# Kernel tuning notes

Hardware: AMD Instinct MI355X
Metric: run time of the kernel (lower is better)

Reference implementation:

```python
import jax, jax.numpy as jnp
import numpy as np

B, N, D = 2, 2048, 1024
H = 16
HD = D // H  # 64
ROPE_BASE = 10000.0


def setup_inputs() -> dict:
    key = jax.random.key(0)
    ks = jax.random.split(key, 5)
    s = 0.02
    return {
        "x": jax.random.normal(ks[0], (B, N, D), dtype=jnp.float32),
        "qkv_w": jax.random.normal(ks[1], (3 * D, D), dtype=jnp.float32) * s,
        "qkv_b": jax.random.normal(ks[2], (3 * D,), dtype=jnp.float32) * s,
        "proj_w": jax.random.normal(ks[3], (D, D), dtype=jnp.float32) * s,
        "proj_b": jax.random.normal(ks[4], (D,), dtype=jnp.float32) * s,
    }


def _rotate_half(t):
    # interleaved pairs: (x1,x2) -> (-x2,x1), matching lucidrains RotaryEmbedding
    t = t.reshape(*t.shape[:-1], -1, 2)
    x1, x2 = t[..., 0], t[..., 1]
    return jnp.stack((-x2, x1), axis=-1).reshape(*t.shape[:-2], -1)


def _apply_rope(t, cos, sin):
    # t: [B, H, N, HD]; cos/sin: [N, HD]
    return t * cos + _rotate_half(t) * sin


def reference(x, qkv_w, qkv_b, proj_w, proj_b):
    b, n, d = x.shape
    scale = HD ** -0.5

    qkv = x @ qkv_w.T + qkv_b                      # [B, N, 3D]
    qkv = qkv.reshape(b, n, 3, H, HD)
    qkv = jnp.transpose(qkv, (2, 0, 3, 1, 4))       # [3, B, H, N, HD]
    q, k, v = qkv[0], qkv[1], qkv[2]

    # RoPE (lang freqs, interpolate_factor=1)
    inv_freq = 1.0 / (ROPE_BASE ** (jnp.arange(0, HD, 2, dtype=jnp.float32) / HD))
    freqs = jnp.arange(n, dtype=jnp.float32)[:, None] * inv_freq[None, :]  # [N, HD/2]
    freqs = jnp.repeat(freqs, 2, axis=-1)           # [N, HD] interleaved
    cos, sin = jnp.cos(freqs), jnp.sin(freqs)
    q = _apply_rope(q, cos, sin)
    k = _apply_rope(k, cos, sin)

    scores = jnp.einsum('bhid,bhjd->bhij', q, k) * scale  # [B, H, N, N]
    causal = jnp.triu(jnp.ones((n, n), dtype=bool), k=1)
    scores = jnp.where(causal, -jnp.inf, scores)
    attn = jax.nn.softmax(scores, axis=-1)

    out = jnp.einsum('bhij,bhjd->bhid', attn, v)    # [B, H, N, HD]
    out = jnp.transpose(out, (0, 2, 1, 3)).reshape(b, n, d)
    return out @ proj_w.T + proj_b
```

## Files before the change

### kernel.cpp

```cpp
#include <hip/hip_runtime.h>
#include <hip/hip_bf16.h>
#include <cstdint>
#include <cstddef>

typedef __hip_bfloat16 bf16;
typedef short bf16x8 __attribute__((ext_vector_type(8)));
typedef float f32x4 __attribute__((ext_vector_type(4)));
typedef float f32x16 __attribute__((ext_vector_type(16)));
typedef int i32x4 __attribute__((ext_vector_type(4)));

#define MFMA16(a, b, c) __builtin_amdgcn_mfma_f32_16x16x32_bf16((a), (b), (c), 0, 0, 0)
#define MFMA32(a, b, c) __builtin_amdgcn_mfma_f32_32x32x16_bf16((a), (b), (c), 0, 0, 0)

__device__ __forceinline__ void glds16(const bf16* g, bf16* l)
{
    __builtin_amdgcn_global_load_lds(
        (const __attribute__((address_space(1))) void*)g,
        (__attribute__((address_space(3))) void*)l, 16, 0, 0);
}

__device__ __forceinline__ unsigned pkbf16(float a, float b)
{
    bf16 ba = __float2bfloat16(a), bb = __float2bfloat16(b);
    unsigned ua = *reinterpret_cast<unsigned short*>(&ba);
    unsigned ub = *reinterpret_cast<unsigned short*>(&bb);
    return ua | (ub << 16);
}

__global__ void cvt_f32_bf16(const float* __restrict__ in, bf16* __restrict__ out, int n4)
{
    int i = blockIdx.x * blockDim.x + threadIdx.x;
    if (i >= n4) return;
    float4 v = *reinterpret_cast<const float4*>(in + (size_t)i * 4);
    __align__(8) bf16 tmp[4];
    tmp[0] = __float2bfloat16(v.x);
    tmp[1] = __float2bfloat16(v.y);
    tmp[2] = __float2bfloat16(v.z);
    tmp[3] = __float2bfloat16(v.w);
    *reinterpret_cast<short4*>(out + (size_t)i * 4) = *reinterpret_cast<short4*>(tmp);
}

__global__ void rope_table_kernel(float2* __restrict__ tab)
{
    int i = blockIdx.x * blockDim.x + threadIdx.x;
    int pos = i >> 5, f = i & 31;
    float inv = powf(10000.f, -(float)f * (1.f / 32.f));
    float ang = (float)pos * inv;
    tab[i] = make_float2(cosf(ang), sinf(ang));
}

__global__ void rope_apply_kernel(bf16* __restrict__ qkv, const float2* __restrict__ tab)
{
    int idx = blockIdx.x * blockDim.x + threadIdx.x;
    int row = idx >> 8;
    int cc  = (idx & 255) * 8;
    int pos = row & 2047;
    int hd  = cc & 63;
    bf16* p = qkv + (size_t)row * 3072 + cc;
    i32x4 v = *reinterpret_cast<const i32x4*>(p);
    bf16* e = reinterpret_cast<bf16*>(&v);
    const float2* tb = tab + pos * 32 + (hd >> 1);
#pragma unroll
    for (int pp = 0; pp < 4; ++pp) {
        float2 cs = tb[pp];
        float x1 = __bfloat162float(e[2 * pp]);
        float x2 = __bfloat162float(e[2 * pp + 1]);
        e[2 * pp]     = __float2bfloat16(x1 * cs.x - x2 * cs.y);
        e[2 * pp + 1] = __float2bfloat16(x2 * cs.x + x1 * cs.y);
    }
    *reinterpret_cast<i32x4*>(p) = v;
}

__device__ inline void store_out(float* p, float v) { *p = v; }
__device__ inline void store_out(bf16* p, float v) { *p = __float2bfloat16(v); }

template <typename OutT>
__global__ void gemm_bt_kernel(const bf16* __restrict__ A, const bf16* __restrict__ BT,
                               const float* __restrict__ bias, OutT* __restrict__ C,
                               int M, int N, int K)
{
    constexpr int BM = 128, BN = 128, BK = 32;
    __shared__ __align__(16) bf16 Al[BM * BK];
    __shared__ __align__(16) bf16 Bl[BN * BK];

    const int tid = threadIdx.x;
    const int l = tid & 63;
    const int w = tid >> 6;
    const int wr = w >> 1, wc = w & 1;
    const int l15 = l & 15, lhi = l >> 4;
    const int row0 = blockIdx.x * BM, col0 = blockIdx.y * BN;

    const int ar0 = tid >> 2, ar1 = (tid + 256) >> 2;
    const int ac  = (tid & 3) * 8;
    const bf16* Ag0 = A + (size_t)(row0 + ar0) * K + ac;
    const bf16* Ag1 = A + (size_t)(row0 + ar1) * K + ac;
    const bf16* Bg0 = BT + (size_t)(col0 + ar0) * K + ac;
    const bf16* Bg1 = BT + (size_t)(col0 + ar1) * K + ac;
    const int wbase = (tid & 192) * 8;
    bf16* sA0 = &Al[wbase];
    bf16* sA1 = &Al[2048 + wbase];
    bf16* sB0 = &Bl[wbase];
    bf16* sB1 = &Bl[2048 + wbase];

    f32x4 acc[4][4] = {};

    for (int k0 = 0; k0 < K; k0 += BK) {
        __syncthreads();
        glds16(Ag0 + k0, sA0);
        glds16(Ag1 + k0, sA1);
        glds16(Bg0 + k0, sB0);
        glds16(Bg1 + k0, sB1);
        __syncthreads();
        bf16x8 af[4], bfr[4];
#pragma unroll
        for (int m = 0; m < 4; ++m)
            af[m] = *reinterpret_cast<const bf16x8*>(&Al[(wr * 64 + m * 16 + l15) * BK + lhi * 8]);
#pragma unroll
        for (int n = 0; n < 4; ++n)
            bfr[n] = *reinterpret_cast<const bf16x8*>(&Bl[(wc * 64 + n * 16 + l15) * BK + lhi * 8]);
#pragma unroll
        for (int m = 0; m < 4; ++m)
#pragma unroll
            for (int n = 0; n < 4; ++n)
                acc[m][n] = MFMA16(af[m], bfr[n], acc[m][n]);
    }

#pragma unroll
    for (int m = 0; m < 4; ++m) {
#pragma unroll
        for (int n = 0; n < 4; ++n) {
            int col = col0 + wc * 64 + n * 16 + l15;
            float bs = bias[col];
#pragma unroll
            for (int j = 0; j < 4; ++j) {
                int row = row0 + wr * 64 + m * 16 + lhi * 4 + j;
                store_out(&C[(size_t)row * N + col], acc[m][n][j] + bs);
            }
        }
    }
}

__global__ __launch_bounds__(128, 2)
void attn_kernel(const bf16* __restrict__ qkv, bf16* __restrict__ outp)
{
    constexpr int LDK = 68, LDV = 68;
    __shared__ __align__(16) bf16 Kl[2][64 * LDK];
    __shared__ __align__(16) bf16 Vt[2][64 * LDV];
    __shared__ float wred[2][32];

    const int bh = blockIdx.x;
    const int b = bh >> 4, h = bh & 15;
    const int q0b = (31 - (int)blockIdx.y) * 64;
    const int tid = threadIdx.x;
    const int w = tid >> 6, l = tid & 63;
    const int q31 = l & 31, hi = l >> 5;
    const int q0w = q0b + w * 32;
    const int qa = q0w + q31;

    const size_t RS = 3072;
    const bf16* base = qkv + (size_t)b * 2048 * RS;

    bf16x8 qf[4];
    {
        const bf16* qr = base + (size_t)qa * RS + h * 64 + hi * 8;
#pragma unroll
        for (int s = 0; s < 4; ++s) {
            bf16x8 v = *reinterpret_cast<const bf16x8*>(qr + s * 16);
            bf16* e = reinterpret_cast<bf16*>(&v);
#pragma unroll
            for (int j = 0; j < 8; ++j)
                e[j] = __float2bfloat16(__bfloat162float(e[j]) * 0.18033688f);
            qf[s] = v;
        }
    }

    const int kr  = tid >> 2;
    const int kc  = (tid & 3) * 16;
    const bf16* kp = base + (size_t)kr * RS + 1024 + h * 64 + kc;
    const bf16* vp = base + (size_t)(w * 32) * RS + 2048 + h * 64 + l;

    i32x4 ka0, ka1, ka2, ka3;
    __align__(16) bf16 vt32[32];

    ka0 = *reinterpret_cast<const i32x4*>(kp);
    ka1 = *reinterpret_cast<const i32x4*>(kp + 8);
    ka2 = *reinterpret_cast<const i32x4*>(kp + 32 * RS);
    ka3 = *reinterpret_cast<const i32x4*>(kp + 32 * RS + 8);
#pragma unroll
    for (int j = 0; j < 32; ++j) vt32[j] = vp[(size_t)j * RS];
    *reinterpret_cast<i32x4*>(&Kl[0][kr * LDK + kc])            = ka0;
    *reinterpret_cast<i32x4*>(&Kl[0][kr * LDK + kc + 8])        = ka1;
    *reinterpret_cast<i32x4*>(&Kl[0][(kr + 32) * LDK + kc])     = ka2;
    *reinterpret_cast<i32x4*>(&Kl[0][(kr + 32) * LDK + kc + 8]) = ka3;
#pragma unroll
    for (int c = 0; c < 4; ++c)
        *reinterpret_cast<i32x4*>(&Vt[0][l * LDV + w * 32 + c * 8]) =
            *reinterpret_cast<const i32x4*>(&vt32[c * 8]);
    __syncthreads();

    float m_run = -1e30f, l_run = 0.f;
    f32x16 o0 = {}, o1 = {};

    const int ntiles = q0b / 64 + 1;
    int cur = 0;
    for (int t = 0; t < ntiles; ++t) {
        const int kv0 = t * 64;
        const bool pf = (t + 1 < ntiles);
        if (pf) {
            kp += 64 * RS;
            vp += 64 * RS;
            ka0 = *reinterpret_cast<const i32x4*>(kp);
            ka1 = *reinterpret_cast<const i32x4*>(kp + 8);
            ka2 = *reinterpret_cast<const i32x4*>(kp + 32 * RS);
            ka3 = *reinterpret_cast<const i32x4*>(kp + 32 * RS + 8);
#pragma unroll
            for (int j = 0; j < 32; ++j) vt32[j] = vp[(size_t)j * RS];
        }

        if (kv0 <= q0w + 31) {
            const bf16* Kc = &Kl[cur][0];
            const bf16* Vc = &Vt[cur][0];

            f32x16 p0 = {}, p1 = {};
#pragma unroll
            for (int s = 0; s < 4; ++s) {
                bf16x8 kf0 = *reinterpret_cast<const bf16x8*>(&Kc[q31 * LDK + s * 16 + hi * 8]);
                bf16x8 kf1 = *reinterpret_cast<const bf16x8*>(&Kc[(32 + q31) * LDK + s * 16 + hi * 8]);
                p0 = MFMA32(kf0, qf[s], p0);
                p1 = MFMA32(kf1, qf[s], p1);
            }

            if (kv0 + 63 > q0w) {
                const int lim = qa - kv0 - 4 * hi;
#pragma unroll
                for (int r = 0; r < 16; ++r) {
                    const int cr = (r & 3) + 8 * (r >> 2);
                    if (cr > lim)      p0[r] = -1e30f;
                    if (cr + 32 > lim) p1[r] = -1e30f;
                }
            }

            float rm = p0[0];
#pragma unroll
            for (int r = 1; r < 16; ++r) rm = fmaxf(rm, p0[r]);
#pragma unroll
            for (int r = 0; r < 16; ++r) rm = fmaxf(rm, p1[r]);
            rm = fmaxf(rm, __shfl_xor(rm, 32));

            if (!__all(rm - m_run <= 8.0f)) {
                float mnew = fmaxf(m_run, rm);
                float alpha = exp2f(m_run - mnew);
                m_run = mnew;
                l_run *= alpha;
                if (hi == 0) wred[w][q31] = alpha;
#pragma unroll
                for (int g = 0; g < 4; ++g) {
                    f32x4 av = *reinterpret_cast<const f32x4*>(&wred[w][8 * g + 4 * hi]);
#pragma unroll
                    for (int tt = 0; tt < 4; ++tt) {
                        o0[4 * g + tt] *= av[tt];
                        o1[4 * g + tt] *= av[tt];
                    }
                }
            }

            float rsum = 0.f;
#pragma unroll
            for (int r = 0; r < 16; ++r) { p0[r] = exp2f(p0[r] - m_run); rsum += p0[r]; }
#pragma unroll
            for (int r = 0; r < 16; ++r) { p1[r] = exp2f(p1[r] - m_run); rsum += p1[r]; }
            rsum += __shfl_xor(rsum, 32);
            l_run += rsum;

            unsigned A[8], Bv[8];
#pragma unroll
            for (int m = 0; m < 4; ++m) {
                A[m]      = pkbf16(p0[4 * m],     p0[4 * m + 1]);
                Bv[m]     = pkbf16(p0[4 * m + 2], p0[4 * m + 3]);
                A[m + 4]  = pkbf16(p1[4 * m],     p1[4 * m + 1]);
                Bv[m + 4] = pkbf16(p1[4 * m + 2], p1[4 * m + 3]);
            }

#pragma unroll
            for (int ks = 0; ks < 4; ++ks) {
                unsigned sa = hi ? A[2 * ks]  : A[2 * ks + 1];
                unsigned sb = hi ? Bv[2 * ks] : Bv[2 * ks + 1];
                unsigned ra = (unsigned)__shfl_xor((int)sa, 32);
                unsigned rb = (unsigned)__shfl_xor((int)sb, 32);
                union { unsigned u[4]; bf16x8 v; } pa;
                if (hi == 0) { pa.u[0] = A[2 * ks];  pa.u[1] = Bv[2 * ks];  pa.u[2] = ra; pa.u[3] = rb; }
                else         { pa.u[0] = ra; pa.u[1] = rb; pa.u[2] = A[2 * ks + 1]; pa.u[3] = Bv[2 * ks + 1]; }
                bf16x8 vf0 = *reinterpret_cast<const bf16x8*>(&Vc[q31 * LDV + ks * 16 + hi * 8]);
                bf16x8 vf1 = *reinterpret_cast<const bf16x8*>(&Vc[(32 + q31) * LDV + ks * 16 + hi * 8]);
                o0 = MFMA32(pa.v, vf0, o0);
                o1 = MFMA32(pa.v, vf1, o1);
            }
        }

        if (pf) {
            const int nxt = cur ^ 1;
            *reinterpret_cast<i32x4*>(&Kl[nxt][kr * LDK + kc])            = ka0;
            *reinterpret_cast<i32x4*>(&Kl[nxt][kr * LDK + kc + 8])        = ka1;
            *reinterpret_cast<i32x4*>(&Kl[nxt][(kr + 32) * LDK + kc])     = ka2;
            *reinterpret_cast<i32x4*>(&Kl[nxt][(kr + 32) * LDK + kc + 8]) = ka3;
#pragma unroll
            for (int c = 0; c < 4; ++c)
                *reinterpret_cast<i32x4*>(&Vt[nxt][l * LDV + w * 32 + c * 8]) =
                    *reinterpret_cast<const i32x4*>(&vt32[c * 8]);
            __syncthreads();
            cur = nxt;
        }
    }

    if (hi == 0) wred[w][q31] = 1.0f / l_run;
#pragma unroll
    for (int g = 0; g < 4; ++g) {
        f32x4 iv = *reinterpret_cast<const f32x4*>(&wred[w][8 * g + 4 * hi]);
#pragma unroll
        for (int tt = 0; tt < 4; ++tt) {
            const int r = 4 * g + tt;
            const int qrow = q0w + 8 * g + 4 * hi + tt;
            bf16* op = outp + (size_t)(b * 2048 + qrow) * 1024 + h * 64 + q31;
            op[0]  = __float2bfloat16(o0[r] * iv[tt]);
            op[32] = __float2bfloat16(o1[r] * iv[tt]);
        }
    }
}

extern "C" void kernel_launch(void* const* d_in, const int* in_sizes, int n_in,
                              void* d_out, int out_size, void* d_ws, size_t ws_size,
                              hipStream_t stream)
{
    const float* x      = (const float*)d_in[0];
    const float* qkv_w  = (const float*)d_in[1];
    const float* qkv_b  = (const float*)d_in[2];
    const float* proj_w = (const float*)d_in[3];
    const float* proj_b = (const float*)d_in[4];
    float* out = (float*)d_out;

    char* ws = (char*)d_ws;
    bf16* x_bf   = (bf16*)ws;  ws += (size_t)4096 * 1024 * 2;
    bf16* wq_bf  = (bf16*)ws;  ws += (size_t)3072 * 1024 * 2;
    bf16* wp_bf  = (bf16*)ws;  ws += (size_t)1024 * 1024 * 2;
    bf16* qkvbuf = (bf16*)ws;  ws += (size_t)4096 * 3072 * 2;
    bf16* aout   = (bf16*)ws;  ws += (size_t)4096 * 1024 * 2;
    float2* tab  = (float2*)ws;

    cvt_f32_bf16<<<4096, 256, 0, stream>>>(x, x_bf, 1048576);
    cvt_f32_bf16<<<3072, 256, 0, stream>>>(qkv_w, wq_bf, 786432);
    cvt_f32_bf16<<<1024, 256, 0, stream>>>(proj_w, wp_bf, 262144);
    rope_table_kernel<<<256, 256, 0, stream>>>(tab);

    gemm_bt_kernel<bf16><<<dim3(32, 24), 256, 0, stream>>>(x_bf, wq_bf, qkv_b, qkvbuf, 4096, 3072, 1024);
    rope_apply_kernel<<<4096, 256, 0, stream>>>(qkvbuf, tab);
    attn_kernel<<<dim3(32, 32), 128, 0, stream>>>(qkvbuf, aout);
    gemm_bt_kernel<float><<<dim3(32, 8), 256, 0, stream>>>(aout, wp_bf, proj_b, out, 4096, 1024, 1024);
}
```

Baseline: 268.0 us.

## Pre-transpose V into a head-major buffer for vectorized attention loads

Adds a kernel that transposes the V part of the QKV buffer into a per-head [d, n] layout, reusing the x_bf workspace, which is dead after the QKV GEMM. The attention kernel then loads V tiles with 16-byte vector loads instead of 32 strided scalar loads per thread, cutting global load instructions and register pressure in the inner loop. It also removes the per-warp skip of fully masked KV tiles, so both warps now always compute the diagonal tile. The cost is an extra kernel launch and one more read and write pass over V.

```diff
diff --git a/kernel.cpp b/kernel.cpp
--- a/kernel.cpp
+++ b/kernel.cpp
@@ -69,6 +69,35 @@
         e[2 * pp + 1] = __float2bfloat16(x2 * cs.x + x1 * cs.y);
     }
     *reinterpret_cast<i32x4*>(p) = v;
+}
+
+__global__ void transpose_v_kernel(const bf16* __restrict__ qkv, bf16* __restrict__ vt)
+{
+    __shared__ __align__(16) bf16 Tl[64 * 68];
+    const int bid = blockIdx.x;
+    const int bh = bid >> 5, nt = bid & 31;
+    const int b = bh >> 4, h = bh & 15;
+    const int n0 = nt * 64;
+    const int tid = threadIdx.x;
+#pragma unroll
+    for (int cc = 0; cc < 2; ++cc) {
+        int c = tid + cc * 256;
+        int r = c >> 3, d8 = (c & 7) * 8;
+        i32x4 v = *reinterpret_cast<const i32x4*>(
+            qkv + (size_t)(b * 2048 + n0 + r) * 3072 + 2048 + h * 64 + d8);
+        *reinterpret_cast<i32x4*>(&Tl[r * 68 + d8]) = v;
+    }
+    __syncthreads();
+#pragma unroll
+    for (int cc = 0; cc < 2; ++cc) {
+        int c = tid + cc * 256;
+        int d = c >> 3, n8 = (c & 7) * 8;
+        __align__(16) bf16 tmp[8];
+#pragma unroll
+        for (int i = 0; i < 8; ++i) tmp[i] = Tl[(n8 + i) * 68 + d];
+        *reinterpret_cast<i32x4*>(vt + ((size_t)bh * 64 + d) * 2048 + n0 + n8) =
+            *reinterpret_cast<const i32x4*>(tmp);
+    }
 }
 
 __device__ inline void store_out(float* p, float v) { *p = v; }
@@ -141,7 +170,8 @@
 }
 
 __global__ __launch_bounds__(128, 2)
-void attn_kernel(const bf16* __restrict__ qkv, bf16* __restrict__ outp)
+void attn_kernel(const bf16* __restrict__ qkv, const bf16* __restrict__ vt,
+                 bf16* __restrict__ outp)
 {
     constexpr int LDK = 68, LDV = 68;
     __shared__ __align__(16) bf16 Kl[2][64 * LDK];
@@ -177,25 +207,27 @@
     const int kr  = tid >> 2;
     const int kc  = (tid & 3) * 16;
     const bf16* kp = base + (size_t)kr * RS + 1024 + h * 64 + kc;
-    const bf16* vp = base + (size_t)(w * 32) * RS + 2048 + h * 64 + l;
+    const int vd  = tid >> 3;
+    const int vk8 = (tid & 7) * 8;
+    const bf16* vS = vt + ((size_t)bh * 64 + vd) * 2048 + vk8;
 
     i32x4 ka0, ka1, ka2, ka3;
-    __align__(16) bf16 vt32[32];
+    i32x4 vv[4];
 
     ka0 = *reinterpret_cast<const i32x4*>(kp);
     ka1 = *reinterpret_cast<const i32x4*>(kp + 8);
     ka2 = *reinterpret_cast<const i32x4*>(kp + 32 * RS);
     ka3 = *reinterpret_cast<const i32x4*>(kp + 32 * RS + 8);
 #pragma unroll
-    for (int j = 0; j < 32; ++j) vt32[j] = vp[(size_t)j * RS];
+    for (int cc = 0; cc < 4; ++cc)
+        vv[cc] = *reinterpret_cast<const i32x4*>(vS + (size_t)cc * 16 * 2048);
     *reinterpret_cast<i32x4*>(&Kl[0][kr * LDK + kc])            = ka0;
     *reinterpret_cast<i32x4*>(&Kl[0][kr * LDK + kc + 8])        = ka1;
     *reinterpret_cast<i32x4*>(&Kl[0][(kr + 32) * LDK + kc])     = ka2;
     *reinterpret_cast<i32x4*>(&Kl[0][(kr + 32) * LDK + kc + 8]) = ka3;
 #pragma unroll
-    for (int c = 0; c < 4; ++c)
-        *reinterpret_cast<i32x4*>(&Vt[0][l * LDV + w * 32 + c * 8]) =
-            *reinterpret_cast<const i32x4*>(&vt32[c * 8]);
+    for (int cc = 0; cc < 4; ++cc)
+        *reinterpret_cast<i32x4*>(&Vt[0][(vd + cc * 16) * LDV + vk8]) = vv[cc];
     __syncthreads();
 
     float m_run = -1e30f, l_run = 0.f;
@@ -208,16 +240,16 @@
         const bool pf = (t + 1 < ntiles);
         if (pf) {
             kp += 64 * RS;
-            vp += 64 * RS;
             ka0 = *reinterpret_cast<const i32x4*>(kp);
             ka1 = *reinterpret_cast<const i32x4*>(kp + 8);
             ka2 = *reinterpret_cast<const i32x4*>(kp + 32 * RS);
             ka3 = *reinterpret_cast<const i32x4*>(kp + 32 * RS + 8);
 #pragma unroll
-            for (int j = 0; j < 32; ++j) vt32[j] = vp[(size_t)j * RS];
-        }
-
-        if (kv0 <= q0w + 31) {
+            for (int cc = 0; cc < 4; ++cc)
+                vv[cc] = *reinterpret_cast<const i32x4*>(vS + (size_t)cc * 16 * 2048 + kv0 + 64);
+        }
+
+        {
             const bf16* Kc = &Kl[cur][0];
             const bf16* Vc = &Vt[cur][0];
 
@@ -304,9 +336,8 @@
             *reinterpret_cast<i32x4*>(&Kl[nxt][(kr + 32) * LDK + kc])     = ka2;
             *reinterpret_cast<i32x4*>(&Kl[nxt][(kr + 32) * LDK + kc + 8]) = ka3;
 #pragma unroll
-            for (int c = 0; c < 4; ++c)
-                *reinterpret_cast<i32x4*>(&Vt[nxt][l * LDV + w * 32 + c * 8]) =
-                    *reinterpret_cast<const i32x4*>(&vt32[c * 8]);
+            for (int cc = 0; cc < 4; ++cc)
+                *reinterpret_cast<i32x4*>(&Vt[nxt][(vd + cc * 16) * LDV + vk8]) = vv[cc];
             __syncthreads();
             cur = nxt;
         }
@@ -345,6 +376,7 @@
     bf16* qkvbuf = (bf16*)ws;  ws += (size_t)4096 * 3072 * 2;
     bf16* aout   = (bf16*)ws;  ws += (size_t)4096 * 1024 * 2;
     float2* tab  = (float2*)ws;
+    bf16* vt = x_bf;
 
     cvt_f32_bf16<<<4096, 256, 0, stream>>>(x, x_bf, 1048576);
     cvt_f32_bf16<<<3072, 256, 0, stream>>>(qkv_w, wq_bf, 786432);
@@ -353,6 +385,7 @@
 
     gemm_bt_kernel<bf16><<<dim3(32, 24), 256, 0, stream>>>(x_bf, wq_bf, qkv_b, qkvbuf, 4096, 3072, 1024);
     rope_apply_kernel<<<4096, 256, 0, stream>>>(qkvbuf, tab);
-    attn_kernel<<<dim3(32, 32), 128, 0, stream>>>(qkvbuf, aout);
+    transpose_v_kernel<<<1024, 256, 0, stream>>>(qkvbuf, vt);
+    attn_kernel<<<dim3(32, 32), 128, 0, stream>>>(qkvbuf, vt, aout);
     gemm_bt_kernel<float><<<dim3(32, 8), 256, 0, stream>>>(aout, wp_bf, proj_b, out, 4096, 1024, 1024);
 }
```

Measured after the change: 250.4 us. -6.6%, faster.
